# Performance work log

Measured on AMD Instinct MI355X. Metric: run time of the kernel, lower is better.

## Reference

```python
import jax, jax.numpy as jnp
import numpy as np

C = 201        # n_classes + 1 (background)
K = 5          # prototypes per class
DIM = 768
B = 64
HP = 16        # patch grid side, n_patches = HP*HP
N_PATCH = HP * HP
GAMMA = 0.999
SK_ITERS = 3
EPS = 1e-12


def setup_inputs() -> dict:
    key = jax.random.key(0)
    k1, k2, k3, k4 = jax.random.split(key, 4)
    return dict(
        patch_tokens=jax.random.normal(k1, (B, N_PATCH, DIM), jnp.float32),
        prototypes=jax.random.normal(k2, (C, K, DIM), jnp.float32) * 0.02,  # trunc_normal(std=0.02) approx
        sa=jnp.full((C - 1, K), 0.5, jnp.float32),                          # sa_init=0.5
        scale=jnp.float32(4.0),                                             # scale_init=4.0
        labels=jax.random.randint(k3, (B,), 0, C - 1),                      # image-level labels in [0, 200)
        masks=jax.random.bernoulli(k4, 0.5, (B, HP, HP)),                   # fg_extractor output
    )


def _masked_sinkhorn(L, m, n_iters=SK_ITERS):
    """Sinkhorn-Knopp over a masked subset of rows.
    L: [N, K] logits, m: [N] bool row mask. Rows outside m stay zero.
    Equivalent to running SK on the gathered rows L[m] (softmax init,
    alternating column/row normalization)."""
    Q = jax.nn.softmax(L, axis=-1) * m[:, None]

    def body(Q, _):
        Q = Q / (Q.sum(axis=0, keepdims=True) + EPS)                         # column normalize
        Q = jnp.where(m[:, None], Q / (Q.sum(axis=1, keepdims=True) + EPS), 0.0)  # row normalize (masked rows)
        return Q, None

    Q, _ = jax.lax.scan(body, Q, None, length=n_iters)
    return Q


def reference(patch_tokens, prototypes, sa, scale, labels, masks):
    # --- cosine patch-prototype logits ---
    tok = patch_tokens / (jnp.linalg.norm(patch_tokens, axis=-1, keepdims=True) + EPS)
    pro = prototypes / (jnp.linalg.norm(prototypes, axis=-1, keepdims=True) + EPS)
    patch_prototype_logits = jnp.einsum('bnd,ckd->bnck', tok, pro)           # [B, N, C, K]

    # --- avg pooling over patches ---
    image_prototype_logits = patch_prototype_logits.mean(axis=1)             # [B, C, K]

    # --- 'sa' classification head ---
    sa_w = jax.nn.softmax(sa, axis=-1) * K                                   # [C-1, K]
    class_logits = (scale * image_prototype_logits[:, :-1, :] * sa_w).sum(-1)  # [B, C-1]

    # --- pseudo patch labels from fg masks ---
    pseudo_patch_labels = jnp.where(masks, labels[:, None, None], C - 1)     # [B, H, W] int
    pl_flat = pseudo_patch_labels.reshape(-1)                                # [B*N]

    # --- online clustering (operates on detached values in the original) ---
    tok_flat = jax.lax.stop_gradient(tok).reshape(-1, DIM)                   # [B*N, D]
    L_flat = jax.lax.stop_gradient(patch_prototype_logits).reshape(-1, C, K)  # [B*N, C, K]
    class_mask = pl_flat[None, :] == jnp.arange(C)[:, None]                  # [C, B*N]

    # vectorized per-class masked Sinkhorn-Knopp (replaces dynamic python loop over unique labels)
    Q_all = jax.vmap(_masked_sinkhorn, in_axes=(1, 0))(L_flat, class_mask)   # [C, B*N, K]

    # prototype candidates: P_c_new = L_c_assignment^T @ I_c (masked rows are zero)
    P_new_c = jnp.einsum('cnk,nd->ckd', Q_all, tok_flat)                     # [C, K, D]
    has_class = class_mask.any(axis=1)[:, None, None]
    new_prototypes = jnp.where(has_class,
                               GAMMA * prototypes + (1.0 - GAMMA) * P_new_c,
                               prototypes)

    # part assignment: argmax over K, gathered at each patch's own class
    idx_all = jnp.argmax(Q_all, axis=-1)                                     # [C, B*N]
    part_assignment_maps = idx_all[pl_flat, jnp.arange(pl_flat.shape[0])].reshape(B, N_PATCH)

    return (patch_prototype_logits, image_prototype_logits, class_logits,
            part_assignment_maps, new_prototypes, pseudo_patch_labels)
```

## Files before the change

### kernel.cpp

```cpp
#include <hip/hip_runtime.h>
#include <math.h>

#define NTOK 16384
#define NPRO 1005
#define DIMD 768
#define CKD  1005
#define CC   201
#define KKp  5
#define BGC  200
#define KEXP 2304
#define KA   1536
#define NPAD 1024

#define OUT_LOGITS   0
#define OUT_IMG      16465920
#define OUT_CLS      (OUT_IMG + 64320)
#define OUT_PART     (OUT_CLS + 12800)
#define OUT_NEWPROTO (OUT_PART + 16384)
#define OUT_PSEUDO   (OUT_NEWPROTO + 771840)

#define WOFF_PACC    0ULL
#define WOFF_A2      3087360ULL
#define WOFF_B2      53419008ULL
#define WOFF_INVTOK  58137600ULL
#define WOFF_PL      58203136ULL
#define WOFF_Q       58268672ULL
#define WOFF_OFFSETS 58596352ULL
#define WOFF_ORDER   58597376ULL

typedef __attribute__((ext_vector_type(8))) short short8;
typedef __attribute__((ext_vector_type(4))) float f32x4;
typedef __attribute__((ext_vector_type(4))) unsigned short usv4;

__device__ __forceinline__ unsigned short f2bf(float x) {
  unsigned int b = __float_as_uint(x);
  unsigned int r = (b + 0x7FFFu + ((b >> 16) & 1u)) >> 16;
  return (unsigned short)r;
}
__device__ __forceinline__ float bf2f(unsigned short u) {
  return __uint_as_float(((unsigned int)u) << 16);
}

__device__ __forceinline__ void async_copy16(const void* g, void* lds) {
  __builtin_amdgcn_global_load_lds(
      (const __attribute__((address_space(1))) unsigned int*)g,
      (__attribute__((address_space(3))) unsigned int*)lds, 16, 0, 0);
}

__global__ __launch_bounds__(256) void conv_kernel(const float* __restrict__ tok,
                                                   const float* __restrict__ pro,
                                                   unsigned short* __restrict__ A2,
                                                   unsigned short* __restrict__ B2,
                                                   float* __restrict__ inv_tok) {
  int wid = (blockIdx.x * 256 + threadIdx.x) >> 6;
  int lane = threadIdx.x & 63;
  if (wid >= NTOK + NPAD) return;

  if (wid < NTOK) {
    const float4* s4 = (const float4*)(tok + (size_t)wid * DIMD);
    float4 v[3];
    float s = 0.0f;
#pragma unroll
    for (int p = 0; p < 3; ++p) {
      v[p] = s4[p * 64 + lane];
      s += v[p].x * v[p].x + v[p].y * v[p].y + v[p].z * v[p].z + v[p].w * v[p].w;
    }
#pragma unroll
    for (int off = 32; off; off >>= 1) s += __shfl_xor(s, off, 64);
    float inv = 1.0f / (sqrtf(s) + 1e-12f);
    if (lane == 0) inv_tok[wid] = inv;
    unsigned short* rowp = A2 + (size_t)wid * KA;
#pragma unroll
    for (int p = 0; p < 3; ++p) {
      float x0 = v[p].x * inv, x1 = v[p].y * inv, x2 = v[p].z * inv, x3 = v[p].w * inv;
      usv4 hi, lo;
      hi.x = f2bf(x0); hi.y = f2bf(x1); hi.z = f2bf(x2); hi.w = f2bf(x3);
      lo.x = f2bf(x0 - bf2f(hi.x)); lo.y = f2bf(x1 - bf2f(hi.y));
      lo.z = f2bf(x2 - bf2f(hi.z)); lo.w = f2bf(x3 - bf2f(hi.w));
      int c = p * 256 + lane * 4;
      *(usv4*)(rowp + c) = hi;
      *(usv4*)(rowp + 768 + c) = lo;
    }
  } else {
    int pw = wid - NTOK;
    unsigned short* rowp = B2 + (size_t)pw * KEXP;
    if (pw >= NPRO) {
      usv4 z = {0, 0, 0, 0};
#pragma unroll
      for (int p = 0; p < 3; ++p) {
        int c = p * 256 + lane * 4;
        *(usv4*)(rowp + c) = z; *(usv4*)(rowp + 768 + c) = z; *(usv4*)(rowp + 1536 + c) = z;
      }
      return;
    }
    const float4* s4 = (const float4*)(pro + (size_t)pw * DIMD);
    float4 v[3];
    float s = 0.0f;
#pragma unroll
    for (int p = 0; p < 3; ++p) {
      v[p] = s4[p * 64 + lane];
      s += v[p].x * v[p].x + v[p].y * v[p].y + v[p].z * v[p].z + v[p].w * v[p].w;
    }
#pragma unroll
    for (int off = 32; off; off >>= 1) s += __shfl_xor(s, off, 64);
    float inv = 1.0f / (sqrtf(s) + 1e-12f);
#pragma unroll
    for (int p = 0; p < 3; ++p) {
      float x0 = v[p].x * inv, x1 = v[p].y * inv, x2 = v[p].z * inv, x3 = v[p].w * inv;
      usv4 hi, lo;
      hi.x = f2bf(x0); hi.y = f2bf(x1); hi.z = f2bf(x2); hi.w = f2bf(x3);
      lo.x = f2bf(x0 - bf2f(hi.x)); lo.y = f2bf(x1 - bf2f(hi.y));
      lo.z = f2bf(x2 - bf2f(hi.z)); lo.w = f2bf(x3 - bf2f(hi.w));
      int c = p * 256 + lane * 4;
      *(usv4*)(rowp + c) = hi;
      *(usv4*)(rowp + 768 + c) = hi;
      *(usv4*)(rowp + 1536 + c) = lo;
    }
  }
}

__global__ __launch_bounds__(1024) void prep_kernel(const void* __restrict__ masks,
                                                    const int* __restrict__ labels,
                                                    int* __restrict__ pl,
                                                    float* __restrict__ out_pseudo,
                                                    int* __restrict__ offsets,
                                                    int* __restrict__ order) {
  __shared__ int hist[256];
  __shared__ int cur[256];
  __shared__ int flagS;
  int t = threadIdx.x;
  int lane = t & 63;
  if (t < 256) hist[t] = 0;
  if (t == 0) flagS = 0;
  __syncthreads();

  const unsigned* mu = (const unsigned*)masks;
  unsigned pr = 0;
  for (int i = t; i < 4096; i += 1024) {
    unsigned v = mu[i];
    if (v == 0x3F800000u)      pr |= 1;
    else if (v > 1u)           pr |= 2;
  }
  if (pr) atomicOr(&flagS, (int)pr);
  __syncthreads();
  int f = flagS;

  int lab[16];
#pragma unroll
  for (int r = 0; r < 16; ++r) {
    int n = r * 1024 + t;
    int m;
    if (f & 1)      m = ((const float*)masks)[n] != 0.0f;
    else if (f & 2) m = ((const unsigned char*)masks)[n] != 0;
    else            m = ((const int*)masks)[n] != 0;
    int l = m ? labels[n >> 8] : BGC;
    lab[r] = l;
    pl[n] = l;
    out_pseudo[n] = (float)l;
    atomicAdd(&hist[l], 1);
  }
  __syncthreads();

  int own = (t < 256) ? hist[t] : 0;
  for (int off = 1; off < 256; off <<= 1) {
    int u = (t >= off && t < 256) ? hist[t - off] : 0;
    __syncthreads();
    if (t < 256) hist[t] += u;
    __syncthreads();
  }
  if (t < 256) {
    int excl = hist[t] - own;
    cur[t] = excl;
    if (t <= CC) offsets[t] = (t < CC) ? excl : hist[CC - 1];
  }
  if (t == CC - 1) offsets[CC] = hist[CC - 1];
  __syncthreads();

#pragma unroll
  for (int r = 0; r < 16; ++r) {
    int n = r * 1024 + t;
    int l = lab[r];
    unsigned long long mk = __ballot(l == BGC);
    if (l == BGC) {
      int rank = __popcll(mk & ((1ull << lane) - 1));
      int leader = (int)(__ffsll((long long)mk) - 1);
      int base = 0;
      if (lane == leader) base = atomicAdd(&cur[BGC], (int)__popcll(mk));
      base = __shfl(base, leader, 64);
      order[base + rank] = n;
    } else {
      order[atomicAdd(&cur[l], 1)] = n;
    }
  }
}

__global__ __launch_bounds__(256, 2) void gemm_kernel(const unsigned short* __restrict__ A2,
                                                      const unsigned short* __restrict__ B2,
                                                      float* __restrict__ C,
                                                      float* __restrict__ img) {
  __shared__ unsigned short As[2][4096];
  __shared__ unsigned short Bs[2][4096];
  const int tid = threadIdx.x;
  const int lane = tid & 63, wave = tid >> 6;
  const int m0 = blockIdx.x * 128, n0 = blockIdx.y * 128;
  const int wr = wave >> 1, wc = wave & 1;

  f32x4 acc[4][4];
#pragma unroll
  for (int i = 0; i < 4; ++i)
#pragma unroll
    for (int j = 0; j < 4; ++j) acc[i][j] = (f32x4){0.f, 0.f, 0.f, 0.f};

  const int r4 = lane >> 2;
  const int kc = (lane & 3) * 8;

  auto STAGE = [&](int buf, int kt) {
    int kb = kt * 32;
    int acol = (kb < KA ? kb : kb - KA) + kc;
    int bcol = kb + kc;
#pragma unroll
    for (int j = 0; j < 2; ++j) {
      int seg = wave * 2 + j;
      async_copy16(A2 + (size_t)(m0 + seg * 16 + r4) * KA + acol, &As[buf][seg * 512]);
      async_copy16(B2 + (size_t)(n0 + seg * 16 + r4) * KEXP + bcol, &Bs[buf][seg * 512]);
    }
  };

  STAGE(0, 0);
  __syncthreads();

  const int rb = wr * 64 + (lane & 15);
  const int cb = wc * 64 + (lane & 15);
  const int hi8 = (lane >> 4) * 8;

  int cur = 0;
  for (int kt = 0; kt < 72; ++kt) {
    if (kt < 71) STAGE(cur ^ 1, kt + 1);
    short8 a[4], b[4];
#pragma unroll
    for (int ff = 0; ff < 4; ++ff) {
      a[ff] = *(const short8*)&As[cur][(rb + ff * 16) * 32 + hi8];
      b[ff] = *(const short8*)&Bs[cur][(cb + ff * 16) * 32 + hi8];
    }
#pragma unroll
    for (int fm = 0; fm < 4; ++fm)
#pragma unroll
      for (int fn = 0; fn < 4; ++fn)
        acc[fm][fn] = __builtin_amdgcn_mfma_f32_16x16x32_bf16(a[fm], b[fn], acc[fm][fn], 0, 0, 0);
    __syncthreads();
    cur ^= 1;
  }

  const int bimg = m0 >> 8;
#pragma unroll
  for (int fn = 0; fn < 4; ++fn) {
    int col = n0 + wc * 64 + fn * 16 + (lane & 15);
    float s = 0.0f;
#pragma unroll
    for (int fm = 0; fm < 4; ++fm) {
      int row = m0 + wr * 64 + fm * 16 + (lane >> 4) * 4;
      f32x4 v = acc[fm][fn];
      if (col < NPRO) {
        C[(size_t)(row + 0) * CKD + col] = v.x;
        C[(size_t)(row + 1) * CKD + col] = v.y;
        C[(size_t)(row + 2) * CKD + col] = v.z;
        C[(size_t)(row + 3) * CKD + col] = v.w;
      }
      s += v.x + v.y + v.z + v.w;
    }
    s += __shfl_xor(s, 16, 64);
    s += __shfl_xor(s, 32, 64);
    if (lane < 16 && col < NPRO)
      atomicAdd(&img[bimg * CKD + col], s * (1.0f / 256.0f));
  }
}

__global__ __launch_bounds__(256) void cls_kernel(const float* __restrict__ img,
                                                  const float* __restrict__ sa,
                                                  const float* __restrict__ scale,
                                                  float* __restrict__ out_cls) {
  int gid = blockIdx.x * 256 + threadIdx.x;
  if (gid >= 64 * 200) return;
  int b = gid / 200, c = gid - b * 200;
  float s5[KKp];
  float mx = -1e30f;
#pragma unroll
  for (int k = 0; k < KKp; ++k) { s5[k] = sa[c * KKp + k]; mx = fmaxf(mx, s5[k]); }
  float den = 0.0f;
#pragma unroll
  for (int k = 0; k < KKp; ++k) { s5[k] = expf(s5[k] - mx); den += s5[k]; }
  float acc = 0.0f;
#pragma unroll
  for (int k = 0; k < KKp; ++k)
    acc += img[(size_t)b * CKD + c * KKp + k] * (s5[k] / den * 5.0f);
  out_cls[gid] = scale[0] * acc;
}

__global__ __launch_bounds__(256) void qsink_kernel(const float* __restrict__ L,
                                                    const int* __restrict__ order,
                                                    const int* __restrict__ offsets,
                                                    float* __restrict__ Q,
                                                    float* __restrict__ out_part) {
  int c = blockIdx.x;
  int s0 = offsets[c], e0 = offsets[c + 1];
  if (s0 >= e0) return;
  int t = threadIdx.x;
  int lane = t & 63, w = t >> 6;
  __shared__ float cs[KKp];
  __shared__ float wsum[4][KKp];

  for (int i = s0 + t; i < e0; i += 256) {
    int n = order[i];
    const float* Lr = L + (size_t)n * CKD + c * KKp;
    float q[KKp];
    float mx = -1e30f;
#pragma unroll
    for (int k = 0; k < KKp; ++k) { q[k] = Lr[k]; mx = fmaxf(mx, q[k]); }
    float den = 0.0f;
#pragma unroll
    for (int k = 0; k < KKp; ++k) { q[k] = expf(q[k] - mx); den += q[k]; }
    float inv = 1.0f / den;
#pragma unroll
    for (int k = 0; k < KKp; ++k) Q[(size_t)n * KKp + k] = q[k] * inv;
  }
  __syncthreads();

  for (int it = 0; it < 3; ++it) {
    float a[KKp] = {0, 0, 0, 0, 0};
    for (int i = s0 + t; i < e0; i += 256) {
      int n = order[i];
      const float* q = Q + (size_t)n * KKp;
#pragma unroll
      for (int k = 0; k < KKp; ++k) a[k] += q[k];
    }
#pragma unroll
    for (int off = 32; off; off >>= 1)
#pragma unroll
      for (int k = 0; k < KKp; ++k) a[k] += __shfl_xor(a[k], off, 64);
    if (lane == 0) {
#pragma unroll
      for (int k = 0; k < KKp; ++k) wsum[w][k] = a[k];
    }
    __syncthreads();
    if (t == 0) {
#pragma unroll
      for (int k = 0; k < KKp; ++k)
        cs[k] = wsum[0][k] + wsum[1][k] + wsum[2][k] + wsum[3][k];
    }
    __syncthreads();

    for (int i = s0 + t; i < e0; i += 256) {
      int n = order[i];
      float q[KKp];
      float r = 0.0f;
#pragma unroll
      for (int k = 0; k < KKp; ++k) {
        q[k] = Q[(size_t)n * KKp + k] / (cs[k] + 1e-12f);
        r += q[k];
      }
      float rinv = 1.0f / (r + 1e-12f);
#pragma unroll
      for (int k = 0; k < KKp; ++k) {
        q[k] *= rinv;
        Q[(size_t)n * KKp + k] = q[k];
      }
      if (it == 2) {
        float best = q[0];
        int bi = 0;
#pragma unroll
        for (int k = 1; k < KKp; ++k)
          if (q[k] > best) { best = q[k]; bi = k; }
        out_part[n] = (float)bi;
      }
    }
    __syncthreads();
  }
}

__global__ __launch_bounds__(256) void pnew_kernel(const int* __restrict__ order,
                                                   const int* __restrict__ pl,
                                                   const float* __restrict__ Q,
                                                   const float* __restrict__ tok,
                                                   const float* __restrict__ inv_tok,
                                                   float* __restrict__ P_acc) {
  __shared__ int idx[32], cls[32];
  int t = threadIdx.x;
  int p0 = blockIdx.x * 32;
  if (t < 32) {
    int n = order[p0 + t];
    idx[t] = n;
    cls[t] = pl[n];
  }
  __syncthreads();
  float acc[KKp][3];
#pragma unroll
  for (int k = 0; k < KKp; ++k)
#pragma unroll
    for (int s = 0; s < 3; ++s) acc[k][s] = 0.0f;
  int cur = cls[0];
  for (int i = 0; i < 32; ++i) {
    int c = cls[i];
    if (c != cur) {
#pragma unroll
      for (int k = 0; k < KKp; ++k)
#pragma unroll
        for (int s = 0; s < 3; ++s) {
          atomicAdd(&P_acc[((size_t)cur * KKp + k) * DIMD + s * 256 + t], acc[k][s]);
          acc[k][s] = 0.0f;
        }
      cur = c;
    }
    int n = idx[i];
    float it = inv_tok[n];
    float q[KKp];
#pragma unroll
    for (int k = 0; k < KKp; ++k) q[k] = Q[(size_t)n * KKp + k];
#pragma unroll
    for (int s = 0; s < 3; ++s) {
      float v = tok[(size_t)n * DIMD + s * 256 + t] * it;
#pragma unroll
      for (int k = 0; k < KKp; ++k) acc[k][s] = fmaf(q[k], v, acc[k][s]);
    }
  }
#pragma unroll
  for (int k = 0; k < KKp; ++k)
#pragma unroll
    for (int s = 0; s < 3; ++s)
      atomicAdd(&P_acc[((size_t)cur * KKp + k) * DIMD + s * 256 + t], acc[k][s]);
}

__global__ __launch_bounds__(256) void newproto_kernel(const float* __restrict__ proto,
                                                       const float* __restrict__ P_acc,
                                                       const int* __restrict__ offsets,
                                                       float* __restrict__ outp) {
  int gid = blockIdx.x * 256 + threadIdx.x;
  if (gid >= CC * KKp * DIMD) return;
  int c = gid / (KKp * DIMD);
  float p = proto[gid];
  bool has = offsets[c + 1] > offsets[c];
  outp[gid] = has ? (0.999f * p + 0.001f * P_acc[gid]) : p;
}

extern "C" void kernel_launch(void* const* d_in, const int* in_sizes, int n_in,
                              void* d_out, int out_size, void* d_ws, size_t ws_size,
                              hipStream_t stream) {
  const float* patch_tokens = (const float*)d_in[0];
  const float* prototypes   = (const float*)d_in[1];
  const float* sa           = (const float*)d_in[2];
  const float* scale        = (const float*)d_in[3];
  const int*   labels       = (const int*)d_in[4];
  const void*  masks        = (const void*)d_in[5];

  float* out = (float*)d_out;
  float* out_logits  = out + OUT_LOGITS;
  float* out_img     = out + OUT_IMG;
  float* out_cls     = out + OUT_CLS;
  float* out_part    = out + OUT_PART;
  float* out_newp    = out + OUT_NEWPROTO;
  float* out_pseudo  = out + OUT_PSEUDO;

  char* w = (char*)d_ws;
  float*          P_acc   = (float*)(w + WOFF_PACC);
  unsigned short* A2      = (unsigned short*)(w + WOFF_A2);
  unsigned short* B2      = (unsigned short*)(w + WOFF_B2);
  float*          inv_tok = (float*)(w + WOFF_INVTOK);
  int*            pl      = (int*)(w + WOFF_PL);
  float*          Q       = (float*)(w + WOFF_Q);
  int*            offsets = (int*)(w + WOFF_OFFSETS);
  int*            order   = (int*)(w + WOFF_ORDER);

  hipMemsetAsync(P_acc, 0, 3087360, stream);
  hipMemsetAsync(out_img, 0, (size_t)64 * CKD * sizeof(float), stream);

  prep_kernel<<<1, 1024, 0, stream>>>(masks, labels, pl, out_pseudo, offsets, order);
  conv_kernel<<<4352, 256, 0, stream>>>(patch_tokens, prototypes, A2, B2, inv_tok);

  gemm_kernel<<<dim3(128, 8), 256, 0, stream>>>(A2, B2, out_logits, out_img);

  cls_kernel<<<50, 256, 0, stream>>>(out_img, sa, scale, out_cls);
  qsink_kernel<<<CC, 256, 0, stream>>>(out_logits, order, offsets, Q, out_part);

  pnew_kernel<<<512, 256, 0, stream>>>(order, pl, Q, patch_tokens, inv_tok, P_acc);
  newproto_kernel<<<3015, 256, 0, stream>>>(prototypes, P_acc, offsets, out_newp);
}
```

Before: 379.7 us.

## Fuse prep and Sinkhorn into one cooperative grid-synced clustering kernel

Replaces the single-block prep kernel and the per-class Sinkhorn kernel with one cooperative kernel of 64 blocks, one per image, with each thread owning a patch. Column sums are computed with block reductions plus global atomics into per-iteration buffers, separated by grid syncs, so Q stays in registers instead of being re-read through the order indirection. Counting, prefix offsets and order scattering are done with ballots and atomics. This removes the serial 1-block prep and the load imbalance of the per-class Sinkhorn blocks, at the cost of four grid-wide barriers and a cooperative launch. The order within each class bucket is no longer deterministic.

Measured after the change: 321.1 us. 1.18x faster.

```diff
diff --git a/kernel.cpp b/kernel.cpp
--- a/kernel.cpp
+++ b/kernel.cpp
@@ -1,5 +1,8 @@
 #include <hip/hip_runtime.h>
+#include <hip/hip_cooperative_groups.h>
 #include <math.h>
+
+namespace cg = cooperative_groups;
 
 #define NTOK 16384
 #define NPRO 1005
@@ -20,13 +23,18 @@
 #define OUT_PSEUDO   (OUT_NEWPROTO + 771840)
 
 #define WOFF_PACC    0ULL
-#define WOFF_A2      3087360ULL
-#define WOFF_B2      53419008ULL
-#define WOFF_INVTOK  58137600ULL
-#define WOFF_PL      58203136ULL
-#define WOFF_Q       58268672ULL
-#define WOFF_OFFSETS 58596352ULL
-#define WOFF_ORDER   58597376ULL
+#define WOFF_COLSUM3 3087360ULL
+#define WOFF_COUNTS  3099648ULL
+#define WOFF_FLAG    3100672ULL
+#define WS_ZERO_B    3100928ULL
+#define WOFF_A2      3100928ULL
+#define WOFF_B2      53432576ULL
+#define WOFF_INVTOK  58151168ULL
+#define WOFF_PL      58216704ULL
+#define WOFF_Q       58282240ULL
+#define WOFF_OFFSETS 58609920ULL
+#define WOFF_CURSORS 58610944ULL
+#define WOFF_ORDER   58611968ULL
 
 typedef __attribute__((ext_vector_type(8))) short short8;
 typedef __attribute__((ext_vector_type(4))) float f32x4;
@@ -119,81 +127,6 @@
   }
 }
 
-__global__ __launch_bounds__(1024) void prep_kernel(const void* __restrict__ masks,
-                                                    const int* __restrict__ labels,
-                                                    int* __restrict__ pl,
-                                                    float* __restrict__ out_pseudo,
-                                                    int* __restrict__ offsets,
-                                                    int* __restrict__ order) {
-  __shared__ int hist[256];
-  __shared__ int cur[256];
-  __shared__ int flagS;
-  int t = threadIdx.x;
-  int lane = t & 63;
-  if (t < 256) hist[t] = 0;
-  if (t == 0) flagS = 0;
-  __syncthreads();
-
-  const unsigned* mu = (const unsigned*)masks;
-  unsigned pr = 0;
-  for (int i = t; i < 4096; i += 1024) {
-    unsigned v = mu[i];
-    if (v == 0x3F800000u)      pr |= 1;
-    else if (v > 1u)           pr |= 2;
-  }
-  if (pr) atomicOr(&flagS, (int)pr);
-  __syncthreads();
-  int f = flagS;
-
-  int lab[16];
-#pragma unroll
-  for (int r = 0; r < 16; ++r) {
-    int n = r * 1024 + t;
-    int m;
-    if (f & 1)      m = ((const float*)masks)[n] != 0.0f;
-    else if (f & 2) m = ((const unsigned char*)masks)[n] != 0;
-    else            m = ((const int*)masks)[n] != 0;
-    int l = m ? labels[n >> 8] : BGC;
-    lab[r] = l;
-    pl[n] = l;
-    out_pseudo[n] = (float)l;
-    atomicAdd(&hist[l], 1);
-  }
-  __syncthreads();
-
-  int own = (t < 256) ? hist[t] : 0;
-  for (int off = 1; off < 256; off <<= 1) {
-    int u = (t >= off && t < 256) ? hist[t - off] : 0;
-    __syncthreads();
-    if (t < 256) hist[t] += u;
-    __syncthreads();
-  }
-  if (t < 256) {
-    int excl = hist[t] - own;
-    cur[t] = excl;
-    if (t <= CC) offsets[t] = (t < CC) ? excl : hist[CC - 1];
-  }
-  if (t == CC - 1) offsets[CC] = hist[CC - 1];
-  __syncthreads();
-
-#pragma unroll
-  for (int r = 0; r < 16; ++r) {
-    int n = r * 1024 + t;
-    int l = lab[r];
-    unsigned long long mk = __ballot(l == BGC);
-    if (l == BGC) {
-      int rank = __popcll(mk & ((1ull << lane) - 1));
-      int leader = (int)(__ffsll((long long)mk) - 1);
-      int base = 0;
-      if (lane == leader) base = atomicAdd(&cur[BGC], (int)__popcll(mk));
-      base = __shfl(base, leader, 64);
-      order[base + rank] = n;
-    } else {
-      order[atomicAdd(&cur[l], 1)] = n;
-    }
-  }
-}
-
 __global__ __launch_bounds__(256, 2) void gemm_kernel(const unsigned short* __restrict__ A2,
                                                       const unsigned short* __restrict__ B2,
                                                       float* __restrict__ C,
@@ -296,85 +229,142 @@
   out_cls[gid] = scale[0] * acc;
 }
 
-__global__ __launch_bounds__(256) void qsink_kernel(const float* __restrict__ L,
-                                                    const int* __restrict__ order,
-                                                    const int* __restrict__ offsets,
-                                                    float* __restrict__ Q,
-                                                    float* __restrict__ out_part) {
-  int c = blockIdx.x;
-  int s0 = offsets[c], e0 = offsets[c + 1];
-  if (s0 >= e0) return;
-  int t = threadIdx.x;
-  int lane = t & 63, w = t >> 6;
-  __shared__ float cs[KKp];
-  __shared__ float wsum[4][KKp];
-
-  for (int i = s0 + t; i < e0; i += 256) {
-    int n = order[i];
-    const float* Lr = L + (size_t)n * CKD + c * KKp;
-    float q[KKp];
-    float mx = -1e30f;
-#pragma unroll
-    for (int k = 0; k < KKp; ++k) { q[k] = Lr[k]; mx = fmaxf(mx, q[k]); }
-    float den = 0.0f;
-#pragma unroll
-    for (int k = 0; k < KKp; ++k) { q[k] = expf(q[k] - mx); den += q[k]; }
-    float inv = 1.0f / den;
-#pragma unroll
-    for (int k = 0; k < KKp; ++k) Q[(size_t)n * KKp + k] = q[k] * inv;
-  }
+__global__ __launch_bounds__(256) void cluster_kernel(const void* __restrict__ masks,
+                                                      const int* __restrict__ labels,
+                                                      const float* __restrict__ L,
+                                                      float* __restrict__ Q,
+                                                      int* __restrict__ pl,
+                                                      float* __restrict__ out_pseudo,
+                                                      float* __restrict__ out_part,
+                                                      int* __restrict__ counts,
+                                                      int* __restrict__ offsets,
+                                                      int* __restrict__ cursors,
+                                                      int* __restrict__ order,
+                                                      float* __restrict__ colsum3,
+                                                      int* __restrict__ flag) {
+  cg::grid_group g = cg::this_grid();
+  const int b = blockIdx.x, t = threadIdx.x;
+  const int n = b * 256 + t;
+  const int lane = t & 63, w = t >> 6;
+
+  __shared__ int wcnt[4];
+  __shared__ int sbase[2];
+  __shared__ float red[4][2 * KKp];
+  __shared__ int sc[256];
+
+  if (t < 64) {
+    unsigned v = ((const unsigned*)masks)[b * 64 + t];
+    unsigned pr = (v == 0x3F800000u) ? 1u : (v > 1u ? 2u : 0u);
+    if (pr) atomicOr(flag, (int)pr);
+  }
+  g.sync();
+  int f = __hip_atomic_load(flag, __ATOMIC_RELAXED, __HIP_MEMORY_SCOPE_AGENT);
+
+  int m;
+  if (f & 1)      m = ((const float*)masks)[n] != 0.0f;
+  else if (f & 2) m = ((const unsigned char*)masks)[n] != 0;
+  else            m = ((const int*)masks)[n] != 0;
+  const int cf = labels[b];
+  const int lab = m ? cf : BGC;
+  pl[n] = lab;
+  out_pseudo[n] = (float)lab;
+
+  unsigned long long mk = __ballot(m != 0);
+  int rkw_fg = __popcll(mk & ((1ull << lane) - 1));
+  int rkw_bg = lane - rkw_fg;
+  if (lane == 0) wcnt[w] = __popcll(mk);
   __syncthreads();
+  int fg_before = 0;
+#pragma unroll
+  for (int i = 0; i < 4; ++i) fg_before += (i < w) ? wcnt[i] : 0;
+  int nf = wcnt[0] + wcnt[1] + wcnt[2] + wcnt[3];
+  int fgrank = fg_before + rkw_fg;
+  int bgrank = (w * 64 - fg_before) + rkw_bg;
+  if (t == 0) {
+    atomicAdd(&counts[cf], nf);
+    atomicAdd(&counts[BGC], 256 - nf);
+  }
+
+  const float* Lr = L + (size_t)n * CKD + lab * KKp;
+  float q[KKp];
+  float mx = -1e30f;
+#pragma unroll
+  for (int k = 0; k < KKp; ++k) { q[k] = Lr[k]; mx = fmaxf(mx, q[k]); }
+  float den = 0.0f;
+#pragma unroll
+  for (int k = 0; k < KKp; ++k) { q[k] = expf(q[k] - mx); den += q[k]; }
+  float inv = 1.0f / den;
+#pragma unroll
+  for (int k = 0; k < KKp; ++k) q[k] *= inv;
 
   for (int it = 0; it < 3; ++it) {
-    float a[KKp] = {0, 0, 0, 0, 0};
-    for (int i = s0 + t; i < e0; i += 256) {
-      int n = order[i];
-      const float* q = Q + (size_t)n * KKp;
-#pragma unroll
-      for (int k = 0; k < KKp; ++k) a[k] += q[k];
-    }
-#pragma unroll
-    for (int off = 32; off; off >>= 1)
-#pragma unroll
-      for (int k = 0; k < KKp; ++k) a[k] += __shfl_xor(a[k], off, 64);
+    float fgv[KKp], bgv[KKp];
+#pragma unroll
+    for (int k = 0; k < KKp; ++k) { fgv[k] = m ? q[k] : 0.0f; bgv[k] = m ? 0.0f : q[k]; }
+#pragma unroll
+    for (int off = 32; off; off >>= 1) {
+#pragma unroll
+      for (int k = 0; k < KKp; ++k) {
+        fgv[k] += __shfl_xor(fgv[k], off, 64);
+        bgv[k] += __shfl_xor(bgv[k], off, 64);
+      }
+    }
     if (lane == 0) {
 #pragma unroll
-      for (int k = 0; k < KKp; ++k) wsum[w][k] = a[k];
+      for (int k = 0; k < KKp; ++k) { red[w][k] = fgv[k]; red[w][KKp + k] = bgv[k]; }
     }
     __syncthreads();
-    if (t == 0) {
-#pragma unroll
-      for (int k = 0; k < KKp; ++k)
-        cs[k] = wsum[0][k] + wsum[1][k] + wsum[2][k] + wsum[3][k];
-    }
-    __syncthreads();
-
-    for (int i = s0 + t; i < e0; i += 256) {
-      int n = order[i];
-      float q[KKp];
-      float r = 0.0f;
-#pragma unroll
-      for (int k = 0; k < KKp; ++k) {
-        q[k] = Q[(size_t)n * KKp + k] / (cs[k] + 1e-12f);
-        r += q[k];
+    if (t < 2 * KKp) {
+      float s = red[0][t] + red[1][t] + red[2][t] + red[3][t];
+      int cls_ = (t < KKp) ? cf : BGC;
+      int kk = (t < KKp) ? t : t - KKp;
+      atomicAdd(&colsum3[it * 1024 + cls_ * KKp + kk], s);
+    }
+    g.sync();
+
+    if (it == 0 && b == 0) {
+      int v0 = (t < CC) ? counts[t] : 0;
+      sc[t] = v0;
+      __syncthreads();
+      for (int off = 1; off < 256; off <<= 1) {
+        int u = (t >= off) ? sc[t - off] : 0;
+        __syncthreads();
+        sc[t] += u;
+        __syncthreads();
       }
-      float rinv = 1.0f / (r + 1e-12f);
-#pragma unroll
-      for (int k = 0; k < KKp; ++k) {
-        q[k] *= rinv;
-        Q[(size_t)n * KKp + k] = q[k];
-      }
-      if (it == 2) {
-        float best = q[0];
-        int bi = 0;
-#pragma unroll
-        for (int k = 1; k < KKp; ++k)
-          if (q[k] > best) { best = q[k]; bi = k; }
-        out_part[n] = (float)bi;
-      }
-    }
-    __syncthreads();
-  }
+      if (t < CC) { offsets[t] = sc[t] - v0; cursors[t] = sc[t] - v0; }
+      if (t == CC - 1) offsets[CC] = sc[t];
+    }
+
+    float r = 0.0f;
+#pragma unroll
+    for (int k = 0; k < KKp; ++k) {
+      q[k] = q[k] / (colsum3[it * 1024 + lab * KKp + k] + 1e-12f);
+      r += q[k];
+    }
+    float rinv = 1.0f / (r + 1e-12f);
+#pragma unroll
+    for (int k = 0; k < KKp; ++k) q[k] *= rinv;
+  }
+
+  float* Qr = Q + (size_t)n * KKp;
+  float best = q[0];
+  int bi = 0;
+#pragma unroll
+  for (int k = 0; k < KKp; ++k) {
+    Qr[k] = q[k];
+    if (k > 0 && q[k] > best) { best = q[k]; bi = k; }
+  }
+  out_part[n] = (float)bi;
+
+  if (t == 0) {
+    sbase[0] = atomicAdd(&cursors[cf], nf);
+    sbase[1] = atomicAdd(&cursors[BGC], 256 - nf);
+  }
+  __syncthreads();
+  int base = m ? sbase[0] : sbase[1];
+  int rank = m ? fgrank : bgrank;
+  order[base + rank] = n;
 }
 
 __global__ __launch_bounds__(256) void pnew_kernel(const int* __restrict__ order,
@@ -461,24 +451,38 @@
 
   char* w = (char*)d_ws;
   float*          P_acc   = (float*)(w + WOFF_PACC);
+  float*          colsum3 = (float*)(w + WOFF_COLSUM3);
+  int*            counts  = (int*)(w + WOFF_COUNTS);
+  int*            flag    = (int*)(w + WOFF_FLAG);
   unsigned short* A2      = (unsigned short*)(w + WOFF_A2);
   unsigned short* B2      = (unsigned short*)(w + WOFF_B2);
   float*          inv_tok = (float*)(w + WOFF_INVTOK);
   int*            pl      = (int*)(w + WOFF_PL);
   float*          Q       = (float*)(w + WOFF_Q);
   int*            offsets = (int*)(w + WOFF_OFFSETS);
+  int*            cursors = (int*)(w + WOFF_CURSORS);
   int*            order   = (int*)(w + WOFF_ORDER);
 
-  hipMemsetAsync(P_acc, 0, 3087360, stream);
+  hipMemsetAsync(d_ws, 0, WS_ZERO_B, stream);
   hipMemsetAsync(out_img, 0, (size_t)64 * CKD * sizeof(float), stream);
 
-  prep_kernel<<<1, 1024, 0, stream>>>(masks, labels, pl, out_pseudo, offsets, order);
   conv_kernel<<<4352, 256, 0, stream>>>(patch_tokens, prototypes, A2, B2, inv_tok);
 
   gemm_kernel<<<dim3(128, 8), 256, 0, stream>>>(A2, B2, out_logits, out_img);
 
   cls_kernel<<<50, 256, 0, stream>>>(out_img, sa, scale, out_cls);
-  qsink_kernel<<<CC, 256, 0, stream>>>(out_logits, order, offsets, Q, out_part);
+
+  {
+    const void* masks_a = masks; const int* labels_a = labels;
+    const float* L_a = out_logits; float* Q_a = Q;
+    int* pl_a = pl; float* pseudo_a = out_pseudo; float* part_a = out_part;
+    int* counts_a = counts; int* offsets_a = offsets; int* cursors_a = cursors;
+    int* order_a = order; float* colsum3_a = colsum3; int* flag_a = flag;
+    void* cargs[] = {&masks_a, &labels_a, &L_a, &Q_a, &pl_a, &pseudo_a, &part_a,
+                     &counts_a, &offsets_a, &cursors_a, &order_a, &colsum3_a, &flag_a};
+    hipLaunchCooperativeKernel((const void*)cluster_kernel, dim3(64), dim3(256),
+                               cargs, 0, stream);
+  }
 
   pnew_kernel<<<512, 256, 0, stream>>>(order, pl, Q, patch_tokens, inv_tok, P_acc);
   newproto_kernel<<<3015, 256, 0, stream>>>(prototypes, P_acc, offsets, out_newp);
```
